# Performance work log

Measured on AMD Instinct MI355X. Metric: run time of the kernel, lower is better.

Reference implementation:

```python
import jax, jax.numpy as jnp
import numpy as np

B, S, D = 2, 2048, 1024
H, A = 16, 64  # num_heads, attention_dim


def setup_inputs() -> dict:
    key = jax.random.key(0)
    ks = jax.random.split(key, 9)
    sd = D ** -0.5
    so = (H * A) ** -0.5
    return {
        "x": jax.random.normal(ks[0], (B, S, D), dtype=jnp.float32),
        "Wq": jax.random.normal(ks[1], (D, H * A), dtype=jnp.float32) * sd,
        "bq": jnp.zeros((H * A,), dtype=jnp.float32),
        "Wk": jax.random.normal(ks[2], (D, H * A), dtype=jnp.float32) * sd,
        "bk": jnp.zeros((H * A,), dtype=jnp.float32),
        "Wv": jax.random.normal(ks[3], (D, H * A), dtype=jnp.float32) * sd,
        "bv": jnp.zeros((H * A,), dtype=jnp.float32),
        "Wo": jax.random.normal(ks[4], (H * A, D), dtype=jnp.float32) * so,
        "bo": jnp.zeros((D,), dtype=jnp.float32),
    }


def reference(x, Wq, bq, Wk, bk, Wv, bv, Wo, bo):
    b, s, _ = x.shape
    # project and split heads: [b, s, H, A]
    q = (x @ Wq + bq).reshape(b, s, H, A)
    k = (x @ Wk + bk).reshape(b, s, H, A)
    v = (x @ Wv + bv).reshape(b, s, H, A)
    # scores [b, H, s, s]
    scores = jnp.einsum("bqhd,bkhd->bhqk", q, k) / jnp.sqrt(jnp.float32(A))
    weights = jax.nn.softmax(scores, axis=-1)
    attended = jnp.einsum("bhqk,bkhd->bqhd", weights, v).reshape(b, s, H * A)
    return attended @ Wo + bo
```

## Files before the change

kernel.cpp:

```cpp
#include <hip/hip_runtime.h>
#include <hip/hip_bf16.h>

typedef __attribute__((ext_vector_type(8))) short bf16x8;
typedef __attribute__((ext_vector_type(4))) float f32x4;

#define LOG2E 1.44269504088896f

extern "C" __device__ float __ocml_native_exp2_f32(float);

__device__ __forceinline__ unsigned short f2bf(float f) {
    union { float f; unsigned int u; } v; v.f = f;
    unsigned int r = v.u + 0x7FFF + ((v.u >> 16) & 1);
    return (unsigned short)(r >> 16);
}

__device__ __forceinline__ unsigned int pk_bf16(float lo, float hi) {
    unsigned int r;
    asm("v_cvt_pk_bf16_f32 %0, %1, %2" : "=v"(r) : "v"(lo), "v"(hi));
    return r;
}

typedef __attribute__((address_space(3))) unsigned int lds_uint;
typedef __attribute__((address_space(1))) const unsigned int glob_uint;
__device__ __forceinline__ void gl2lds16(const void* g, void* l) {
    __builtin_amdgcn_global_load_lds((glob_uint*)g, (lds_uint*)l, 16, 0, 0);
}

__global__ __launch_bounds__(256) void cvt_bf16(const float* __restrict__ in,
                                                unsigned int* __restrict__ out, int n4) {
    int i = blockIdx.x * 256 + threadIdx.x;
    if (i >= n4) return;
    float4 v = ((const float4*)in)[i];
    uint2 o;
    o.x = pk_bf16(v.x, v.y);
    o.y = pk_bf16(v.z, v.w);
    ((uint2*)out)[i] = o;
}

__global__ __launch_bounds__(256) void transpose4_bf16(
    const float* __restrict__ w0, const float* __restrict__ w1,
    const float* __restrict__ w2, const float* __restrict__ w3,
    unsigned short* __restrict__ o0, unsigned short* __restrict__ o1,
    unsigned short* __restrict__ o2, unsigned short* __restrict__ o3) {
    const int z = blockIdx.z;
    const float* in = (z == 0) ? w0 : (z == 1) ? w1 : (z == 2) ? w2 : w3;
    unsigned short* out = (z == 0) ? o0 : (z == 1) ? o1 : (z == 2) ? o2 : o3;
    __shared__ float t[32][33];
    int tx = threadIdx.x & 31, ty = threadIdx.x >> 5;
    int r0 = blockIdx.y * 32, c0 = blockIdx.x * 32;
    for (int i = 0; i < 32; i += 8)
        t[ty + i][tx] = in[(size_t)(r0 + ty + i) * 1024 + c0 + tx];
    __syncthreads();
    for (int i = 0; i < 32; i += 8)
        out[(size_t)(c0 + ty + i) * 1024 + r0 + tx] = f2bf(t[tx][ty + i]);
}

__device__ __forceinline__ void gemm_core(const short* __restrict__ A,
                                          const short* __restrict__ BT,
                                          int K, int bm0, int bn0,
                                          short* As, short* Bs, f32x4 acc[4][4]) {
    const int tid = threadIdx.x;
    const int lane = tid & 63;
    const int w = tid >> 6;
    const int wr0 = (w >> 1) * 64;
    const int wc0 = (w & 1) * 64;
    const int l15 = lane & 15, quad = lane >> 4;
    const int sr = lane >> 2;
    const int slog = (lane & 3) ^ (sr & 3);

    for (int i = 0; i < 4; i++)
        for (int j = 0; j < 4; j++) acc[i][j] = (f32x4)0.f;

    for (int k0 = 0; k0 < K; k0 += 32) {
        for (int i = 0; i < 4; i++) {
            int c = w * 4 + i;
            if (c < 8)
                gl2lds16(A + (size_t)(bm0 + c * 16 + sr) * K + k0 + slog * 8,
                         As + c * 512);
            else
                gl2lds16(BT + (size_t)(bn0 + (c - 8) * 16 + sr) * K + k0 + slog * 8,
                         Bs + (c - 8) * 512);
        }
        __syncthreads();
        const int ph = (quad ^ (l15 & 3)) * 8;
        bf16x8 af[4], bfr[4];
        for (int im = 0; im < 4; im++)
            af[im] = *(const bf16x8*)&As[(wr0 + im * 16 + l15) * 32 + ph];
        for (int in = 0; in < 4; in++)
            bfr[in] = *(const bf16x8*)&Bs[(wc0 + in * 16 + l15) * 32 + ph];
        for (int im = 0; im < 4; im++)
            for (int in = 0; in < 4; in++)
                acc[im][in] = __builtin_amdgcn_mfma_f32_16x16x32_bf16(af[im], bfr[in], acc[im][in], 0, 0, 0);
        __syncthreads();
    }
}

__global__ __launch_bounds__(256) void gemm_qkv(
    const short* __restrict__ xb,
    const short* __restrict__ wqT, const short* __restrict__ wkT, const short* __restrict__ wvT,
    const float* __restrict__ bq, const float* __restrict__ bk, const float* __restrict__ bv,
    unsigned short* __restrict__ qb, unsigned short* __restrict__ kb, unsigned short* __restrict__ vTb) {
    __shared__ short As[4096], Bs[4096];
    const int z = blockIdx.z;
    const short* Amat = (z == 2) ? wvT : xb;
    const short* Bmat = (z == 0) ? wqT : (z == 1) ? wkT : xb;
    const float* bias = (z == 0) ? bq : (z == 1) ? bk : bv;
    const float scl = (z == 0) ? 0.125f * LOG2E : 1.f;
    const int bm0 = (z == 2) ? blockIdx.y * 128 : blockIdx.x * 128;
    const int bn0 = (z == 2) ? blockIdx.x * 128 : blockIdx.y * 128;
    f32x4 acc[4][4];
    gemm_core(Amat, Bmat, 1024, bm0, bn0, As, Bs, acc);
    const int lane = threadIdx.x & 63, w = threadIdx.x >> 6;
    const int wr0 = (w >> 1) * 64, wc0 = (w & 1) * 64, l15 = lane & 15, quad = lane >> 4;
    if (z == 2) {
        for (int im = 0; im < 4; im++)
            for (int in = 0; in < 4; in++)
                for (int r = 0; r < 4; r++) {
                    int rowa = bm0 + wr0 + im * 16 + quad * 4 + r;
                    int colg = bn0 + wc0 + in * 16 + l15;
                    unsigned short ov = f2bf(acc[im][in][r] + bias[rowa]);
                    int b = colg >> 11, s = colg & 2047;
                    vTb[(size_t)b * 2097152 + (size_t)rowa * 2048 + s] = ov;
                }
    } else {
        for (int im = 0; im < 4; im++)
            for (int in = 0; in < 4; in++)
                for (int r = 0; r < 4; r++) {
                    int rowg = bm0 + wr0 + im * 16 + quad * 4 + r;
                    int colg = bn0 + wc0 + in * 16 + l15;
                    unsigned short ov = f2bf((acc[im][in][r] + bias[colg]) * scl);
                    int b = rowg >> 11, s = rowg & 2047;
                    int h = colg >> 6, a = colg & 63;
                    int bh = b * 16 + h;
                    if (z == 0) qb[((size_t)bh * 2048 + s) * 64 + a] = ov;
                    else        kb[((size_t)bh * 2048 + s) * 64 + a] = ov;
                }
    }
}

__global__ __launch_bounds__(256) void gemm_out(
    const short* __restrict__ att, const short* __restrict__ woT,
    const float* __restrict__ bo, float* __restrict__ out) {
    __shared__ short As[4096], Bs[4096];
    const int bm0 = blockIdx.x * 128, bn0 = blockIdx.y * 128;
    f32x4 acc[4][4];
    gemm_core(att, woT, 1024, bm0, bn0, As, Bs, acc);
    const int lane = threadIdx.x & 63, w = threadIdx.x >> 6;
    const int wr0 = (w >> 1) * 64, wc0 = (w & 1) * 64, l15 = lane & 15, quad = lane >> 4;
    for (int im = 0; im < 4; im++)
        for (int in = 0; in < 4; in++)
            for (int r = 0; r < 4; r++) {
                int rowg = bm0 + wr0 + im * 16 + quad * 4 + r;
                int colg = bn0 + wc0 + in * 16 + l15;
                out[(size_t)rowg * 1024 + colg] = acc[im][in][r] + bo[colg];
            }
}

__global__ __launch_bounds__(512, 4) void flash_attn(
    const unsigned short* __restrict__ qb, const unsigned short* __restrict__ kb,
    const unsigned short* __restrict__ vTb, unsigned short* __restrict__ att) {
    __shared__ short QP[9216];
    __shared__ short Ks[2][4096];
    __shared__ short Vs[2][4096];
    const int tid = threadIdx.x, lane = tid & 63, w = tid >> 6;
    const int l15 = lane & 15, quad = lane >> 4;
    const int q0 = blockIdx.x * 128;
    const int bh = blockIdx.y;
    const size_t qkbase = (size_t)bh * 2048 * 64;
    const size_t vbase = (size_t)bh * 64 * 2048;
    const int sr = lane >> 3;
    const int slog = (lane & 7) ^ sr;
    const int l7 = l15 & 7;

    for (int i = 0; i < 4; i++) {
        int c = w * 4 + i;
        if (c < 16)
            gl2lds16(qb + qkbase + (size_t)(q0 + c * 8 + sr) * 64 + slog * 8, QP + c * 512);
        else if (c < 24)
            gl2lds16(kb + qkbase + (size_t)((c - 16) * 8 + sr) * 64 + slog * 8,
                     Ks[0] + (c - 16) * 512);
        else
            gl2lds16(vTb + vbase + (size_t)((c - 24) * 8 + sr) * 2048 + slog * 8,
                     Vs[0] + (c - 24) * 512);
    }
    __syncthreads();

    const int wq0 = w * 16;
    const int c0 = (quad ^ l7) * 8, c1 = c0 ^ 32;
    const int fb = l15 * 64;
    bf16x8 aq0 = *(const bf16x8*)&QP[(wq0 + l15) * 64 + c0];
    bf16x8 aq1 = *(const bf16x8*)&QP[(wq0 + l15) * 64 + c1];
    __syncthreads();

    f32x4 o[4];
    for (int dt = 0; dt < 4; dt++) o[dt] = (f32x4)0.f;
    f32x4 ls = (f32x4)0.f;

    short* Pw = QP + w * 16 * 72;
    short* Pst = Pw + l15 * 72 + quad * 4;
    const short* Prd = Pw + l15 * 72 + quad * 8;

    const unsigned short* sgp;
    int sgstep; int sg2;
    const int slo = (w & 3) * 1024;
    if (w < 4) {
        sgp = kb + qkbase + (size_t)(64 + w * 16 + sr) * 64 + slog * 8;
        sgstep = 4096; sg2 = 512;
    } else {
        sgp = vTb + vbase + (size_t)((w - 4) * 16 + sr) * 2048 + 64 + slog * 8;
        sgstep = 64; sg2 = 16384;
    }
    short* sb0 = (w < 4 ? Ks[0] : Vs[0]) + slo;
    short* sb1 = (w < 4 ? Ks[1] : Vs[1]) + slo;

    auto step = [&](const short* Kb, const short* Vb, bool stage,
                    const unsigned short* sg, short* sd) {
        if (stage) {
            gl2lds16(sg, sd);
            gl2lds16(sg + sg2, sd + 512);
        }
        f32x4 sc[4];
#pragma unroll
        for (int t = 0; t < 4; t++) {
            bf16x8 ak = *(const bf16x8*)(Kb + fb + c0 + t * 1024);
            sc[t] = __builtin_amdgcn_mfma_f32_16x16x32_bf16(ak, aq0, (f32x4)0.f, 0, 0, 0);
        }
#pragma unroll
        for (int t = 0; t < 4; t++) {
            bf16x8 ak = *(const bf16x8*)(Kb + fb + c1 + t * 1024);
            sc[t] = __builtin_amdgcn_mfma_f32_16x16x32_bf16(ak, aq1, sc[t], 0, 0, 0);
        }
#pragma unroll
        for (int t = 0; t < 4; t++) {
#pragma unroll
            for (int r = 0; r < 4; r++) sc[t][r] = __ocml_native_exp2_f32(sc[t][r]);
            ls += sc[t];
            uint2 pk;
            pk.x = pk_bf16(sc[t][0], sc[t][1]);
            pk.y = pk_bf16(sc[t][2], sc[t][3]);
            *(uint2*)(Pst + t * 16) = pk;
        }
#pragma unroll
        for (int t2 = 0; t2 < 2; t2++) {
            bf16x8 bp = *(const bf16x8*)(Prd + t2 * 32);
            const int cc = t2 ? c1 : c0;
#pragma unroll
            for (int dt = 0; dt < 4; dt++) {
                bf16x8 av = *(const bf16x8*)(Vb + fb + cc + dt * 1024);
                o[dt] = __builtin_amdgcn_mfma_f32_16x16x32_bf16(av, bp, o[dt], 0, 0, 0);
            }
        }
        __syncthreads();
    };

    for (int kv0 = 0; kv0 < 2048; kv0 += 128) {
        step(Ks[0], Vs[0], true, sgp, sb1);
        sgp += sgstep;
        step(Ks[1], Vs[1], kv0 + 128 < 2048, sgp, sb0);
        sgp += sgstep;
    }

    const int b = bh >> 4, h = bh & 15;
    float l = (ls[0] + ls[1]) + (ls[2] + ls[3]);
    l += __shfl_xor(l, 16);
    l += __shfl_xor(l, 32);
    float inv = 1.f / l;
    int s = q0 + wq0 + l15;
    for (int dt = 0; dt < 4; dt++) {
        uint2 pk;
        pk.x = pk_bf16(o[dt][0] * inv, o[dt][1] * inv);
        pk.y = pk_bf16(o[dt][2] * inv, o[dt][3] * inv);
        int col = h * 64 + dt * 16 + quad * 4;
        *(uint2*)&att[((size_t)b * 2048 + s) * 1024 + col] = pk;
    }
}

extern "C" void kernel_launch(void* const* d_in, const int* in_sizes, int n_in,
                              void* d_out, int out_size, void* d_ws, size_t ws_size,
                              hipStream_t stream) {
    const float* x  = (const float*)d_in[0];
    const float* Wq = (const float*)d_in[1];
    const float* bq = (const float*)d_in[2];
    const float* Wk = (const float*)d_in[3];
    const float* bk = (const float*)d_in[4];
    const float* Wv = (const float*)d_in[5];
    const float* bv = (const float*)d_in[6];
    const float* Wo = (const float*)d_in[7];
    const float* bo = (const float*)d_in[8];
    float* out = (float*)d_out;

    short* ws  = (short*)d_ws;
    short* xb  = ws;
    short* wqT = ws + 4 * 1024 * 1024;
    short* wkT = wqT + 1024 * 1024;
    short* wvT = wkT + 1024 * 1024;
    short* woT = wvT + 1024 * 1024;
    short* qb  = woT + 1024 * 1024;
    short* kb  = qb + 4 * 1024 * 1024;
    short* vTb = kb + 4 * 1024 * 1024;
    short* att = vTb + 4 * 1024 * 1024;

    cvt_bf16<<<4096, 256, 0, stream>>>(x, (unsigned int*)xb, 1024 * 1024);
    transpose4_bf16<<<dim3(32, 32, 4), 256, 0, stream>>>(
        Wq, Wk, Wv, Wo,
        (unsigned short*)wqT, (unsigned short*)wkT,
        (unsigned short*)wvT, (unsigned short*)woT);
    gemm_qkv<<<dim3(32, 8, 3), 256, 0, stream>>>(xb, wqT, wkT, wvT, bq, bk, bv,
                                                 (unsigned short*)qb, (unsigned short*)kb,
                                                 (unsigned short*)vTb);
    flash_attn<<<dim3(16, 32), 512, 0, stream>>>((const unsigned short*)qb,
                                                 (const unsigned short*)kb,
                                                 (const unsigned short*)vTb,
                                                 (unsigned short*)att);
    gemm_out<<<dim3(32, 8), 256, 0, stream>>>(att, woT, bo, out);
}
```

Baseline: 206.3 us.

## Give flash-attn waves two query row tiles and rewrite out-GEMM with 512 threads

Flash attention now runs 4 waves per block instead of 8, and each wave handles 32 query rows as two 16-row sub-tiles. Every K/V fragment read from LDS is therefore reused for two MFMAs, which halves LDS traffic per FLOP, but raises register pressure and cuts wave count per block. Separately, gemm_out drops the shared gemm_core in favor of an inline 512-thread loop with a 32-wide K step and swizzled LDS, where each wave computes a 32x64 tile. This trades more waves for latency hiding against a loop with no double buffering and two barriers per K step.

```diff
diff --git a/kernel.cpp b/kernel.cpp
--- a/kernel.cpp
+++ b/kernel.cpp
@@ -138,16 +138,44 @@
     }
 }
 
-__global__ __launch_bounds__(256) void gemm_out(
+__global__ __launch_bounds__(512, 2) void gemm_out(
     const short* __restrict__ att, const short* __restrict__ woT,
     const float* __restrict__ bo, float* __restrict__ out) {
     __shared__ short As[4096], Bs[4096];
     const int bm0 = blockIdx.x * 128, bn0 = blockIdx.y * 128;
-    f32x4 acc[4][4];
-    gemm_core(att, woT, 1024, bm0, bn0, As, Bs, acc);
-    const int lane = threadIdx.x & 63, w = threadIdx.x >> 6;
-    const int wr0 = (w >> 1) * 64, wc0 = (w & 1) * 64, l15 = lane & 15, quad = lane >> 4;
-    for (int im = 0; im < 4; im++)
+    const int tid = threadIdx.x, lane = tid & 63, w = tid >> 6;
+    const int wr0 = (w >> 1) * 32, wc0 = (w & 1) * 64;
+    const int l15 = lane & 15, quad = lane >> 4;
+    const int sr = lane >> 2;
+    const int slog = (lane & 3) ^ (sr & 3);
+
+    f32x4 acc[2][4];
+    for (int i = 0; i < 2; i++)
+        for (int j = 0; j < 4; j++) acc[i][j] = (f32x4)0.f;
+
+    for (int k0 = 0; k0 < 1024; k0 += 32) {
+        for (int i = 0; i < 2; i++) {
+            int c = w * 2 + i;
+            if (c < 8)
+                gl2lds16(att + (size_t)(bm0 + c * 16 + sr) * 1024 + k0 + slog * 8,
+                         As + c * 512);
+            else
+                gl2lds16(woT + (size_t)(bn0 + (c - 8) * 16 + sr) * 1024 + k0 + slog * 8,
+                         Bs + (c - 8) * 512);
+        }
+        __syncthreads();
+        const int ph = (quad ^ (l15 & 3)) * 8;
+        bf16x8 af[2], bfr[4];
+        for (int im = 0; im < 2; im++)
+            af[im] = *(const bf16x8*)&As[(wr0 + im * 16 + l15) * 32 + ph];
+        for (int in = 0; in < 4; in++)
+            bfr[in] = *(const bf16x8*)&Bs[(wc0 + in * 16 + l15) * 32 + ph];
+        for (int im = 0; im < 2; im++)
+            for (int in = 0; in < 4; in++)
+                acc[im][in] = __builtin_amdgcn_mfma_f32_16x16x32_bf16(af[im], bfr[in], acc[im][in], 0, 0, 0);
+        __syncthreads();
+    }
+    for (int im = 0; im < 2; im++)
         for (int in = 0; in < 4; in++)
             for (int r = 0; r < 4; r++) {
                 int rowg = bm0 + wr0 + im * 16 + quad * 4 + r;
@@ -156,7 +184,7 @@
             }
 }
 
-__global__ __launch_bounds__(512, 4) void flash_attn(
+__global__ __launch_bounds__(256, 2) void flash_attn(
     const unsigned short* __restrict__ qb, const unsigned short* __restrict__ kb,
     const unsigned short* __restrict__ vTb, unsigned short* __restrict__ att) {
     __shared__ short QP[9216];
@@ -172,8 +200,8 @@
     const int slog = (lane & 7) ^ sr;
     const int l7 = l15 & 7;
 
-    for (int i = 0; i < 4; i++) {
-        int c = w * 4 + i;
+    for (int i = 0; i < 8; i++) {
+        int c = w * 8 + i;
         if (c < 16)
             gl2lds16(qb + qkbase + (size_t)(q0 + c * 8 + sr) * 64 + slog * 8, QP + c * 512);
         else if (c < 24)
@@ -185,69 +213,86 @@
     }
     __syncthreads();
 
-    const int wq0 = w * 16;
+    const int wq0 = w * 32;
     const int c0 = (quad ^ l7) * 8, c1 = c0 ^ 32;
     const int fb = l15 * 64;
-    bf16x8 aq0 = *(const bf16x8*)&QP[(wq0 + l15) * 64 + c0];
-    bf16x8 aq1 = *(const bf16x8*)&QP[(wq0 + l15) * 64 + c1];
+    bf16x8 aqA0 = *(const bf16x8*)&QP[(wq0 + l15) * 64 + c0];
+    bf16x8 aqB0 = *(const bf16x8*)&QP[(wq0 + l15) * 64 + c1];
+    bf16x8 aqA1 = *(const bf16x8*)&QP[(wq0 + 16 + l15) * 64 + c0];
+    bf16x8 aqB1 = *(const bf16x8*)&QP[(wq0 + 16 + l15) * 64 + c1];
     __syncthreads();
 
-    f32x4 o[4];
-    for (int dt = 0; dt < 4; dt++) o[dt] = (f32x4)0.f;
-    f32x4 ls = (f32x4)0.f;
-
-    short* Pw = QP + w * 16 * 72;
+    f32x4 o[4][2];
+    for (int dt = 0; dt < 4; dt++)
+        for (int rt = 0; rt < 2; rt++) o[dt][rt] = (f32x4)0.f;
+    f32x4 ls0 = (f32x4)0.f, ls1 = (f32x4)0.f;
+
+    short* Pw = QP + w * 2304;
     short* Pst = Pw + l15 * 72 + quad * 4;
     const short* Prd = Pw + l15 * 72 + quad * 8;
 
     const unsigned short* sgp;
-    int sgstep; int sg2;
-    const int slo = (w & 3) * 1024;
-    if (w < 4) {
-        sgp = kb + qkbase + (size_t)(64 + w * 16 + sr) * 64 + slog * 8;
-        sgstep = 4096; sg2 = 512;
+    int sgcall, sgtile;
+    short *sb0, *sb1;
+    if (w < 2) {
+        sgp = kb + qkbase + (size_t)(64 + w * 32 + sr) * 64 + slog * 8;
+        sgcall = 512;
+        sgtile = 4096;
+        sb0 = Ks[0] + w * 2048; sb1 = Ks[1] + w * 2048;
     } else {
-        sgp = vTb + vbase + (size_t)((w - 4) * 16 + sr) * 2048 + 64 + slog * 8;
-        sgstep = 64; sg2 = 16384;
-    }
-    short* sb0 = (w < 4 ? Ks[0] : Vs[0]) + slo;
-    short* sb1 = (w < 4 ? Ks[1] : Vs[1]) + slo;
+        sgp = vTb + vbase + (size_t)((w - 2) * 32 + sr) * 2048 + 64 + slog * 8;
+        sgcall = 16384;
+        sgtile = 64;
+        sb0 = Vs[0] + (w - 2) * 2048; sb1 = Vs[1] + (w - 2) * 2048;
+    }
 
     auto step = [&](const short* Kb, const short* Vb, bool stage,
                     const unsigned short* sg, short* sd) {
         if (stage) {
-            gl2lds16(sg, sd);
-            gl2lds16(sg + sg2, sd + 512);
-        }
-        f32x4 sc[4];
+#pragma unroll
+            for (int i = 0; i < 4; i++)
+                gl2lds16(sg + (size_t)i * sgcall, sd + i * 512);
+        }
+        f32x4 sc[4][2];
 #pragma unroll
         for (int t = 0; t < 4; t++) {
             bf16x8 ak = *(const bf16x8*)(Kb + fb + c0 + t * 1024);
-            sc[t] = __builtin_amdgcn_mfma_f32_16x16x32_bf16(ak, aq0, (f32x4)0.f, 0, 0, 0);
+            sc[t][0] = __builtin_amdgcn_mfma_f32_16x16x32_bf16(ak, aqA0, (f32x4)0.f, 0, 0, 0);
+            sc[t][1] = __builtin_amdgcn_mfma_f32_16x16x32_bf16(ak, aqA1, (f32x4)0.f, 0, 0, 0);
         }
 #pragma unroll
         for (int t = 0; t < 4; t++) {
             bf16x8 ak = *(const bf16x8*)(Kb + fb + c1 + t * 1024);
-            sc[t] = __builtin_amdgcn_mfma_f32_16x16x32_bf16(ak, aq1, sc[t], 0, 0, 0);
+            sc[t][0] = __builtin_amdgcn_mfma_f32_16x16x32_bf16(ak, aqB0, sc[t][0], 0, 0, 0);
+            sc[t][1] = __builtin_amdgcn_mfma_f32_16x16x32_bf16(ak, aqB1, sc[t][1], 0, 0, 0);
         }
 #pragma unroll
         for (int t = 0; t < 4; t++) {
 #pragma unroll
-            for (int r = 0; r < 4; r++) sc[t][r] = __ocml_native_exp2_f32(sc[t][r]);
-            ls += sc[t];
-            uint2 pk;
-            pk.x = pk_bf16(sc[t][0], sc[t][1]);
-            pk.y = pk_bf16(sc[t][2], sc[t][3]);
-            *(uint2*)(Pst + t * 16) = pk;
+            for (int r = 0; r < 4; r++) {
+                sc[t][0][r] = __ocml_native_exp2_f32(sc[t][0][r]);
+                sc[t][1][r] = __ocml_native_exp2_f32(sc[t][1][r]);
+            }
+            ls0 += sc[t][0];
+            ls1 += sc[t][1];
+            uint2 pk0, pk1;
+            pk0.x = pk_bf16(sc[t][0][0], sc[t][0][1]);
+            pk0.y = pk_bf16(sc[t][0][2], sc[t][0][3]);
+            pk1.x = pk_bf16(sc[t][1][0], sc[t][1][1]);
+            pk1.y = pk_bf16(sc[t][1][2], sc[t][1][3]);
+            *(uint2*)(Pst + t * 16) = pk0;
+            *(uint2*)(Pst + 1152 + t * 16) = pk1;
         }
 #pragma unroll
         for (int t2 = 0; t2 < 2; t2++) {
-            bf16x8 bp = *(const bf16x8*)(Prd + t2 * 32);
+            bf16x8 bp0 = *(const bf16x8*)(Prd + t2 * 32);
+            bf16x8 bp1 = *(const bf16x8*)(Prd + 1152 + t2 * 32);
             const int cc = t2 ? c1 : c0;
 #pragma unroll
             for (int dt = 0; dt < 4; dt++) {
                 bf16x8 av = *(const bf16x8*)(Vb + fb + cc + dt * 1024);
-                o[dt] = __builtin_amdgcn_mfma_f32_16x16x32_bf16(av, bp, o[dt], 0, 0, 0);
+                o[dt][0] = __builtin_amdgcn_mfma_f32_16x16x32_bf16(av, bp0, o[dt][0], 0, 0, 0);
+                o[dt][1] = __builtin_amdgcn_mfma_f32_16x16x32_bf16(av, bp1, o[dt][1], 0, 0, 0);
             }
         }
         __syncthreads();
@@ -255,23 +300,27 @@
 
     for (int kv0 = 0; kv0 < 2048; kv0 += 128) {
         step(Ks[0], Vs[0], true, sgp, sb1);
-        sgp += sgstep;
+        sgp += sgtile;
         step(Ks[1], Vs[1], kv0 + 128 < 2048, sgp, sb0);
-        sgp += sgstep;
+        sgp += sgtile;
     }
 
     const int b = bh >> 4, h = bh & 15;
-    float l = (ls[0] + ls[1]) + (ls[2] + ls[3]);
-    l += __shfl_xor(l, 16);
-    l += __shfl_xor(l, 32);
-    float inv = 1.f / l;
-    int s = q0 + wq0 + l15;
-    for (int dt = 0; dt < 4; dt++) {
-        uint2 pk;
-        pk.x = pk_bf16(o[dt][0] * inv, o[dt][1] * inv);
-        pk.y = pk_bf16(o[dt][2] * inv, o[dt][3] * inv);
-        int col = h * 64 + dt * 16 + quad * 4;
-        *(uint2*)&att[((size_t)b * 2048 + s) * 1024 + col] = pk;
+#pragma unroll
+    for (int rt = 0; rt < 2; rt++) {
+        f32x4 ls = rt ? ls1 : ls0;
+        float l = (ls[0] + ls[1]) + (ls[2] + ls[3]);
+        l += __shfl_xor(l, 16);
+        l += __shfl_xor(l, 32);
+        float inv = 1.f / l;
+        int s = q0 + wq0 + rt * 16 + l15;
+        for (int dt = 0; dt < 4; dt++) {
+            uint2 pk;
+            pk.x = pk_bf16(o[dt][rt][0] * inv, o[dt][rt][1] * inv);
+            pk.y = pk_bf16(o[dt][rt][2] * inv, o[dt][rt][3] * inv);
+            int col = h * 64 + dt * 16 + quad * 4;
+            *(uint2*)&att[((size_t)b * 2048 + s) * 1024 + col] = pk;
+        }
     }
 }
 
@@ -308,9 +357,9 @@
     gemm_qkv<<<dim3(32, 8, 3), 256, 0, stream>>>(xb, wqT, wkT, wvT, bq, bk, bv,
                                                  (unsigned short*)qb, (unsigned short*)kb,
                                                  (unsigned short*)vTb);
-    flash_attn<<<dim3(16, 32), 512, 0, stream>>>((const unsigned short*)qb,
+    flash_attn<<<dim3(16, 32), 256, 0, stream>>>((const unsigned short*)qb,
                                                  (const unsigned short*)kb,
                                                  (const unsigned short*)vTb,
                                                  (unsigned short*)att);
-    gemm_out<<<dim3(32, 8), 256, 0, stream>>>(att, woT, bo, out);
-}
+    gemm_out<<<dim3(32, 8), 512, 0, stream>>>(att, woT, bo, out);
+}
```

New measurement: 208.7 us. No clear change (+1.2%).
